# Kernel optimization log

Measured on AMD Instinct MI355X. Metric: run time of the kernel, lower is better.

The kernel has to match this reference:

```python
import jax, jax.numpy as jnp
import numpy as np
import math

B, S, D_MODEL, H, D_K = 8, 1024, 512, 8, 64


def setup_inputs() -> dict:
    key = jax.random.key(0)
    ks = jax.random.split(key, 12)
    s = 1.0 / math.sqrt(D_MODEL)
    inp = {
        "q": jax.random.normal(ks[0], (B, S, D_MODEL), dtype=jnp.float32),
        "k": jax.random.normal(ks[1], (B, S, D_MODEL), dtype=jnp.float32),
        "v": jax.random.normal(ks[2], (B, S, D_MODEL), dtype=jnp.float32),
        "Wq": jax.random.normal(ks[3], (D_MODEL, D_MODEL), dtype=jnp.float32) * s,
        "bq": jnp.zeros((D_MODEL,), dtype=jnp.float32),
        "Wk": jax.random.normal(ks[4], (D_MODEL, D_MODEL), dtype=jnp.float32) * s,
        "bk": jnp.zeros((D_MODEL,), dtype=jnp.float32),
        "Wv": jax.random.normal(ks[5], (D_MODEL, D_MODEL), dtype=jnp.float32) * s,
        "bv": jnp.zeros((D_MODEL,), dtype=jnp.float32),
        "Wo": jax.random.normal(ks[6], (D_MODEL, D_MODEL), dtype=jnp.float32) * s,
        "bo": jnp.zeros((D_MODEL,), dtype=jnp.float32),
        # xavier_uniform on (H,1,1): bound = sqrt(6/(1+1)) ~ 1.732
        "gammas": jax.random.uniform(ks[7], (H, 1, 1), minval=-1.732, maxval=1.732, dtype=jnp.float32),
        "mask": jnp.triu(jnp.ones((S, S), dtype=bool), k=1),  # mask future positions
        "key_padding_mask": jnp.zeros((B, S), dtype=bool),
    }
    return inp


def reference(q, k, v, Wq, bq, Wk, bk, Wv, bv, Wo, bo, gammas, mask, key_padding_mask):
    bs, seqlen = q.shape[0], q.shape[1]
    NEG = -1e32

    def proj(x, W, b):
        # nn.Linear: x @ W.T + b, then split heads -> [b, h, s, d_k]
        return (x @ W.T + b).reshape(bs, seqlen, H, D_K).transpose(0, 2, 1, 3)

    qh, kh, vh = proj(q, Wq, bq), proj(k, Wk, bk), proj(v, Wv, bv)

    scores = jnp.einsum("bhqd,bhkd->bhqk", qh, kh) / math.sqrt(D_K)
    full_mask = mask[None, None, :, :] | key_padding_mask[:, None, None, :]  # [b,1,s,s] bcast over h

    # --- distance-decay branch (torch.no_grad / detach) ---
    scores_ = jax.nn.softmax(jnp.where(full_mask, NEG, scores), axis=-1)
    scores_ = scores_ * (~full_mask).astype(scores.dtype)
    distcum = jnp.cumsum(scores_, axis=-1)  # forward=True
    disttotal = jnp.sum(scores_, axis=-1, keepdims=True)
    idx = jnp.arange(seqlen)
    position_effect = jnp.abs(idx[None, :] - idx[:, None]).astype(scores.dtype)  # |i-j|
    dist_scores = jnp.sqrt(jnp.clip((disttotal - distcum) * position_effect, 0.0))
    dist_scores = jax.lax.stop_gradient(dist_scores)

    gamma = -jax.nn.softplus(gammas)[None]  # [1, h, 1, 1]
    total_effect = jnp.clip(jnp.exp(dist_scores * gamma), 1e-5, 1e5)

    attn = jax.nn.softmax(jnp.where(full_mask, NEG, scores * total_effect), axis=-1)
    out = jnp.einsum("bhqk,bhkd->bhqd", attn, vh)
    concat = out.transpose(0, 2, 1, 3).reshape(bs, seqlen, D_MODEL)
    return concat @ Wo.T + bo
```

## Files before the change

### kernel.cpp

```cpp
#include <hip/hip_runtime.h>
#include <hip/hip_bf16.h>
#include <math.h>

#define NB   8
#define NS   1024
#define NDM  512
#define NH   8
#define NDK  64
#define NM   8192

typedef __attribute__((ext_vector_type(8))) short short8;
typedef __attribute__((ext_vector_type(4))) float f32x4;

__device__ __forceinline__ unsigned short f2b(float f) {
    __hip_bfloat16 h = __float2bfloat16(f);
    unsigned short u;
    __builtin_memcpy(&u, &h, 2);
    return u;
}
__device__ __forceinline__ float b2f(unsigned short u) {
    return __uint_as_float(((unsigned)u) << 16);
}
__device__ __forceinline__ float exp2_raw(float x) { float r; asm("v_exp_f32 %0, %1" : "=v"(r) : "v"(x)); return r; }
__device__ __forceinline__ float sqrt_raw(float x) { float r; asm("v_sqrt_f32 %0, %1" : "=v"(r) : "v"(x)); return r; }
__device__ __forceinline__ float rcp_raw(float x)  { float r; asm("v_rcp_f32 %0, %1" : "=v"(r) : "v"(x)); return r; }

template<int CTRL, int RM>
__device__ __forceinline__ float dpp_mov0(float x) {
    int m = __builtin_amdgcn_update_dpp(0, __float_as_int(x), CTRL, RM, 0xf, true);
    return __int_as_float(m);
}
__device__ __forceinline__ float wave_incl_scan(float x) {
    x += dpp_mov0<0x111, 0xf>(x);
    x += dpp_mov0<0x112, 0xf>(x);
    x += dpp_mov0<0x114, 0xf>(x);
    x += dpp_mov0<0x118, 0xf>(x);
    x += dpp_mov0<0x142, 0xa>(x);
    x += dpp_mov0<0x143, 0xc>(x);
    return x;
}
__device__ __forceinline__ float lane63(float x) {
    return __int_as_float(__builtin_amdgcn_readlane(__float_as_int(x), 63));
}

__device__ __forceinline__ short8 pack8(float4 a, float4 b) {
    short8 r;
    r[0] = (short)f2b(a.x); r[1] = (short)f2b(a.y);
    r[2] = (short)f2b(a.z); r[3] = (short)f2b(a.w);
    r[4] = (short)f2b(b.x); r[5] = (short)f2b(b.y);
    r[6] = (short)f2b(b.z); r[7] = (short)f2b(b.w);
    return r;
}

__device__ __forceinline__ void gload16(const unsigned short* g, unsigned short* l) {
    __builtin_amdgcn_global_load_lds(
        (const __attribute__((address_space(1))) void*)g,
        (__attribute__((address_space(3))) void*)l, 16, 0, 0);
}

template<int OMODE, bool ACVT, bool BCVT>
__device__ __forceinline__ void gemm_body64(unsigned short* As, unsigned short* Bs,
                                            const void* __restrict__ Ap,
                                            const void* __restrict__ Wp,
                                            const float* __restrict__ bias,
                                            void* __restrict__ outp) {
    const int tid = threadIdx.x, lane = tid & 63, wid = tid >> 6;
    const int l15 = lane & 15, lhi = lane >> 4;
    const int m0 = (blockIdx.x >> 2) * 64;
    const int n0 = (blockIdx.x & 3) * 128;
    const int wr = wid >> 1, wc = wid & 1;
    const float* Af = (const float*)Ap;
    const unsigned short* Ab = (const unsigned short*)Ap;
    const float* Wf = (const float*)Wp;
    const unsigned short* Wb = (const unsigned short*)Wp;

    f32x4 acc[2][4];
#pragma unroll
    for (int i = 0; i < 2; ++i)
#pragma unroll
        for (int j = 0; j < 4; ++j) acc[i][j] = (f32x4){0.f, 0.f, 0.f, 0.f};

    for (int kk0 = 0; kk0 < NDM; kk0 += 64) {
#pragma unroll
        for (int c = 0; c < 2; ++c) {
            int ci = tid + 256 * c, row = ci >> 3, ch = ci & 7;
            int sch = ch ^ (row & 7);
            if (ACVT) {
                const float* p = Af + (size_t)(m0 + row) * NDM + kk0 + ch * 8;
                *(short8*)(As + row * 64 + sch * 8) = pack8(*(const float4*)p, *(const float4*)(p + 4));
            } else {
                gload16(Ab + (size_t)(m0 + row) * NDM + kk0 + sch * 8, As + ci * 8);
            }
        }
#pragma unroll
        for (int c = 0; c < 4; ++c) {
            int ci = tid + 256 * c, row = ci >> 3, ch = ci & 7;
            int sch = ch ^ (row & 7);
            if (BCVT) {
                const float* p = Wf + (size_t)(n0 + row) * NDM + kk0 + ch * 8;
                *(short8*)(Bs + row * 64 + sch * 8) = pack8(*(const float4*)p, *(const float4*)(p + 4));
            } else {
                gload16(Wb + (size_t)(n0 + row) * NDM + kk0 + sch * 8, Bs + ci * 8);
            }
        }
        __syncthreads();
        short8 af[2][2], bf[4][2];
#pragma unroll
        for (int mi = 0; mi < 2; ++mi)
#pragma unroll
            for (int kk = 0; kk < 2; ++kk) {
                int row = wr * 32 + mi * 16 + l15;
                af[mi][kk] = *(const short8*)(As + row * 64 + (((kk * 4 + lhi) ^ (l15 & 7)) << 3));
            }
#pragma unroll
        for (int ni = 0; ni < 4; ++ni)
#pragma unroll
            for (int kk = 0; kk < 2; ++kk) {
                int row = wc * 64 + ni * 16 + l15;
                bf[ni][kk] = *(const short8*)(Bs + row * 64 + (((kk * 4 + lhi) ^ (l15 & 7)) << 3));
            }
#pragma unroll
        for (int mi = 0; mi < 2; ++mi)
#pragma unroll
            for (int ni = 0; ni < 4; ++ni) {
                acc[mi][ni] = __builtin_amdgcn_mfma_f32_16x16x32_bf16(af[mi][0], bf[ni][0], acc[mi][ni], 0, 0, 0);
                acc[mi][ni] = __builtin_amdgcn_mfma_f32_16x16x32_bf16(af[mi][1], bf[ni][1], acc[mi][ni], 0, 0, 0);
            }
        __syncthreads();
    }

#pragma unroll
    for (int mi = 0; mi < 2; ++mi) {
#pragma unroll
        for (int ni = 0; ni < 4; ++ni) {
            int row0 = m0 + wr * 32 + mi * 16 + lhi * 4;
            int col  = n0 + wc * 64 + ni * 16 + l15;
            float bv = bias[col];
            if (OMODE == 0) {
                unsigned short* o = (unsigned short*)outp;
                int h = col >> 6, d = col & 63;
#pragma unroll
                for (int r = 0; r < 4; ++r) {
                    int m = row0 + r;
                    int b = m >> 10, s = m & 1023;
                    o[(size_t)(((b * NH + h) * NS) + s) * NDK + d] = f2b(acc[mi][ni][r] + bv);
                }
            } else if (OMODE == 1) {
                unsigned short* o = (unsigned short*)outp;
                int h = col >> 6, d = col & 63;
                int b = row0 >> 10, s0 = row0 & 1023;
                ushort4 u;
                u.x = f2b(acc[mi][ni][0] + bv);
                u.y = f2b(acc[mi][ni][1] + bv);
                u.z = f2b(acc[mi][ni][2] + bv);
                u.w = f2b(acc[mi][ni][3] + bv);
                *(ushort4*)(o + (size_t)((b * NH + h) * NDK + d) * NS + s0) = u;
            } else {
                float* o = (float*)outp;
#pragma unroll
                for (int r = 0; r < 4; ++r)
                    o[(size_t)(row0 + r) * NDM + col] = acc[mi][ni][r] + bv;
            }
        }
    }
}

__global__ __launch_bounds__(256, 4) void qkv_gemm(const float* __restrict__ q,
                                                   const float* __restrict__ k,
                                                   const float* __restrict__ v,
                                                   const float* __restrict__ Wq,
                                                   const float* __restrict__ Wk,
                                                   const float* __restrict__ Wv,
                                                   const float* __restrict__ bq,
                                                   const float* __restrict__ bk,
                                                   const float* __restrict__ bv,
                                                   unsigned short* __restrict__ Qh,
                                                   unsigned short* __restrict__ Kh,
                                                   unsigned short* __restrict__ Vt) {
    __shared__ unsigned short As[64 * 64];
    __shared__ unsigned short Bs[128 * 64];
    const int y = blockIdx.y;
    if (y == 0)      gemm_body64<0, true, true>(As, Bs, q, Wq, bq, Qh);
    else if (y == 1) gemm_body64<0, true, true>(As, Bs, k, Wk, bk, Kh);
    else             gemm_body64<1, true, true>(As, Bs, v, Wv, bv, Vt);
}

__global__ __launch_bounds__(256, 4) void wo_gemm(const unsigned short* __restrict__ A,
                                                  const float* __restrict__ Wo,
                                                  const float* __restrict__ bo,
                                                  float* __restrict__ out) {
    __shared__ unsigned short As[64 * 64];
    __shared__ unsigned short Bs[128 * 64];
    gemm_body64<2, false, true>(As, Bs, A, Wo, bo, out);
}

template<int EW>
__device__ __forceinline__ void phase2_rows(unsigned short* pb, int r0, int wid,
                                            int lane, float g2) {
    const int cb = lane * EW;
#pragma unroll
    for (int t = 0; t < 4; ++t) {
        const int rr = wid + 4 * t;
        const int i  = r0 + rr;
        unsigned short* rowp = pb + rr * 1024;
        float s[EW];
        if (EW == 8) {
            short8 raw = *(const short8*)(rowp + ((lane ^ rr) << 3));
#pragma unroll
            for (int u = 0; u < 8; ++u) s[u] = b2f((unsigned short)raw[u]);
        } else {
            short8 raw0 = *(const short8*)(rowp + (((2 * lane)     ^ rr) << 3));
            short8 raw1 = *(const short8*)(rowp + (((2 * lane + 1) ^ rr) << 3));
#pragma unroll
            for (int u = 0; u < 8; ++u) {
                s[u]     = b2f((unsigned short)raw0[u]);
                s[(EW == 16 ? 8 : 0) + u] = b2f((unsigned short)raw1[u]);
            }
        }
#pragma unroll
        for (int u = 0; u < EW; ++u)
            if (cb + u > i) s[u] = -1e30f;
        float p[EW];
        float run = 0.f;
#pragma unroll
        for (int u = 0; u < EW; ++u) { run += exp2_raw(s[u]); p[u] = run; }
        const float inc      = wave_incl_scan(run);
        const float l1       = lane63(inc);
        const float invl1    = rcp_raw(l1);
        const float taillane = l1 - (inc - run);
        const float di       = (float)(i - cb);
        float l2 = 0.f;
#pragma unroll
        for (int u = 0; u < EW; ++u) {
            float tail = fmaxf(taillane - p[u], 0.f);
            float t2   = (tail * invl1) * (di - (float)u);
            float te   = fmaxf(exp2_raw(g2 * sqrt_raw(t2)), 1e-5f);
            float w    = exp2_raw(s[u] * te);
            s[u] = w;
            l2 += w;
        }
        const float l2t  = lane63(wave_incl_scan(l2));
        const float inv2 = rcp_raw(l2t);
        if (EW == 8) {
            short8 h;
#pragma unroll
            for (int u = 0; u < 8; ++u) h[u] = (short)f2b(s[u] * inv2);
            *(short8*)(rowp + ((lane ^ rr) << 3)) = h;
        } else {
            short8 h0, h1;
#pragma unroll
            for (int u = 0; u < 8; ++u) {
                h0[u] = (short)f2b(s[u] * inv2);
                h1[u] = (short)f2b(s[(EW == 16 ? 8 : 0) + u] * inv2);
            }
            *(short8*)(rowp + (((2 * lane)     ^ rr) << 3)) = h0;
            *(short8*)(rowp + (((2 * lane + 1) ^ rr) << 3)) = h1;
        }
    }
}

__global__ __launch_bounds__(256, 4) void attn_kernel(const unsigned short* __restrict__ Qh,
                                                      const unsigned short* __restrict__ Kh,
                                                      const unsigned short* __restrict__ Vt,
                                                      const float* __restrict__ gammas,
                                                      unsigned short* __restrict__ concat) {
    __shared__ unsigned short pb[16 * 1024];
    const int bh   = blockIdx.x & 63;
    const int pair = blockIdx.x >> 6;
    const int tid = threadIdx.x, lane = tid & 63, wid = tid >> 6;
    const int l15 = lane & 15, lhi = lane >> 4;
    const float SC = 0.125f * 1.44269504f;

    const unsigned short* Kb = Kh + (size_t)bh * NS * NDK;
    const unsigned short* Vb = Vt + (size_t)bh * NDK * NS;
    const float g  = gammas[bh & (NH - 1)];
    const float g2 = -log1pf(__expf(g)) * 1.44269504f;
    const int bq_ = bh >> 3, hq = bh & 7;

    for (int hs = 0; hs < 2; ++hs) {
        const int qt = hs ? (63 - pair) : pair;
        const int r0 = qt * 16;
        const int C  = ((r0 + 16 + 63) >> 6) << 6;

        const unsigned short* Qb = Qh + (size_t)(bh * NS + r0) * NDK;
        short8 qf0 = *(const short8*)(Qb + l15 * NDK + lhi * 8);
        short8 qf1 = *(const short8*)(Qb + l15 * NDK + lhi * 8 + 32);
        for (int j0 = wid * 16; j0 < C; j0 += 64) {
            const unsigned short* kp = Kb + (size_t)(j0 + l15) * NDK + lhi * 8;
            short8 kf0 = *(const short8*)kp;
            short8 kf1 = *(const short8*)(kp + 32);
            f32x4 a = {0.f, 0.f, 0.f, 0.f};
            a = __builtin_amdgcn_mfma_f32_16x16x32_bf16(kf0, qf0, a, 0, 0, 0);
            a = __builtin_amdgcn_mfma_f32_16x16x32_bf16(kf1, qf1, a, 0, 0, 0);
            ushort4 u;
            u.x = f2b(a[0] * SC);
            u.y = f2b(a[1] * SC);
            u.z = f2b(a[2] * SC);
            u.w = f2b(a[3] * SC);
            int ch = ((j0 >> 3) + (lhi >> 1)) ^ l15;
            *(ushort4*)(pb + l15 * 1024 + ch * 8 + (lhi & 1) * 4) = u;
        }
        __syncthreads();

        if (hs == 0) phase2_rows<8>(pb, r0, wid, lane, g2);
        else         phase2_rows<16>(pb, r0, wid, lane, g2);
        __syncthreads();

        const int d0 = wid * 16;
        f32x4 acc = {0.f, 0.f, 0.f, 0.f};
        for (int j0 = 0; j0 < C; j0 += 32) {
            short8 av = *(const short8*)(Vb + (size_t)(d0 + l15) * NS + j0 + lhi * 8);
            short8 pw = *(const short8*)(pb + l15 * 1024 + (((((j0 >> 3) + lhi)) ^ l15) << 3));
            acc = __builtin_amdgcn_mfma_f32_16x16x32_bf16(av, pw, acc, 0, 0, 0);
        }
        {
            int d = d0 + lhi * 4;
            int s = r0 + l15;
            ushort4 u;
            u.x = f2b(acc[0]); u.y = f2b(acc[1]);
            u.z = f2b(acc[2]); u.w = f2b(acc[3]);
            *(ushort4*)(concat + (size_t)(bq_ * NS + s) * NDM + hq * NDK + d) = u;
        }
        __syncthreads();
    }
}

extern "C" void kernel_launch(void* const* d_in, const int* in_sizes, int n_in,
                              void* d_out, int out_size, void* d_ws, size_t ws_size,
                              hipStream_t stream) {
    const float* q  = (const float*)d_in[0];
    const float* k  = (const float*)d_in[1];
    const float* v  = (const float*)d_in[2];
    const float* Wq = (const float*)d_in[3];
    const float* bq = (const float*)d_in[4];
    const float* Wk = (const float*)d_in[5];
    const float* bk = (const float*)d_in[6];
    const float* Wv = (const float*)d_in[7];
    const float* bv = (const float*)d_in[8];
    const float* Wo = (const float*)d_in[9];
    const float* bo = (const float*)d_in[10];
    const float* gm = (const float*)d_in[11];

    char* w = (char*)d_ws;
    unsigned short* Qh     = (unsigned short*)(w);
    unsigned short* Kh     = (unsigned short*)(w + (size_t)8388608);
    unsigned short* Vt     = (unsigned short*)(w + (size_t)16777216);
    unsigned short* concat = (unsigned short*)(w + (size_t)25165824);

    qkv_gemm<<<dim3(512, 3), dim3(256), 0, stream>>>(q, k, v, Wq, Wk, Wv, bq, bk, bv, Qh, Kh, Vt);
    attn_kernel<<<dim3(2048), dim3(256), 0, stream>>>(Qh, Kh, Vt, gm, concat);
    wo_gemm<<<dim3(512), dim3(256), 0, stream>>>(concat, Wo, bo, (float*)d_out);
}
```

Before: 129.8 us.

## Enlarge GEMM tiles to 128x128 and use truncating bf16 conversion

The projection and output GEMMs move from 64x128 to 128x128 block tiles, so each wave computes a 64x64 sub-tile. This halves the grid and raises operand reuse per LDS load, at the cost of more accumulator registers and lower occupancy. All fp32-to-bf16 conversions switch from round-to-nearest to bit truncation with packed 32-bit stores, which cuts conversion ALU work. Truncation adds a small downward bias and extra rounding error in Q/K/V, the probabilities and concat.

```diff
diff --git a/kernel.cpp b/kernel.cpp
--- a/kernel.cpp
+++ b/kernel.cpp
@@ -12,11 +12,11 @@
 typedef __attribute__((ext_vector_type(8))) short short8;
 typedef __attribute__((ext_vector_type(4))) float f32x4;
 
-__device__ __forceinline__ unsigned short f2b(float f) {
-    __hip_bfloat16 h = __float2bfloat16(f);
-    unsigned short u;
-    __builtin_memcpy(&u, &h, 2);
-    return u;
+__device__ __forceinline__ unsigned int pack2t(float lo, float hi) {
+    return (__float_as_uint(hi) & 0xffff0000u) | (__float_as_uint(lo) >> 16);
+}
+__device__ __forceinline__ unsigned short f2bt(float f) {
+    return (unsigned short)(__float_as_uint(f) >> 16);
 }
 __device__ __forceinline__ float b2f(unsigned short u) {
     return __uint_as_float(((unsigned)u) << 16);
@@ -43,12 +43,15 @@
     return __int_as_float(__builtin_amdgcn_readlane(__float_as_int(x), 63));
 }
 
-__device__ __forceinline__ short8 pack8(float4 a, float4 b) {
-    short8 r;
-    r[0] = (short)f2b(a.x); r[1] = (short)f2b(a.y);
-    r[2] = (short)f2b(a.z); r[3] = (short)f2b(a.w);
-    r[4] = (short)f2b(b.x); r[5] = (short)f2b(b.y);
-    r[6] = (short)f2b(b.z); r[7] = (short)f2b(b.w);
+__device__ __forceinline__ uint4 pack8t(const float* p) {
+    const unsigned int* u = (const unsigned int*)p;
+    uint4 a = *(const uint4*)u;
+    uint4 b = *(const uint4*)(u + 4);
+    uint4 r;
+    r.x = (a.y & 0xffff0000u) | (a.x >> 16);
+    r.y = (a.w & 0xffff0000u) | (a.z >> 16);
+    r.z = (b.y & 0xffff0000u) | (b.x >> 16);
+    r.w = (b.w & 0xffff0000u) | (b.z >> 16);
     return r;
 }
 
@@ -59,14 +62,14 @@
 }
 
 template<int OMODE, bool ACVT, bool BCVT>
-__device__ __forceinline__ void gemm_body64(unsigned short* As, unsigned short* Bs,
-                                            const void* __restrict__ Ap,
-                                            const void* __restrict__ Wp,
-                                            const float* __restrict__ bias,
-                                            void* __restrict__ outp) {
+__device__ __forceinline__ void gemm_body128(unsigned short* As, unsigned short* Bs,
+                                             const void* __restrict__ Ap,
+                                             const void* __restrict__ Wp,
+                                             const float* __restrict__ bias,
+                                             void* __restrict__ outp) {
     const int tid = threadIdx.x, lane = tid & 63, wid = tid >> 6;
     const int l15 = lane & 15, lhi = lane >> 4;
-    const int m0 = (blockIdx.x >> 2) * 64;
+    const int m0 = (blockIdx.x >> 2) * 128;
     const int n0 = (blockIdx.x & 3) * 128;
     const int wr = wid >> 1, wc = wid & 1;
     const float* Af = (const float*)Ap;
@@ -74,20 +77,20 @@
     const float* Wf = (const float*)Wp;
     const unsigned short* Wb = (const unsigned short*)Wp;
 
-    f32x4 acc[2][4];
-#pragma unroll
-    for (int i = 0; i < 2; ++i)
+    f32x4 acc[4][4];
+#pragma unroll
+    for (int i = 0; i < 4; ++i)
 #pragma unroll
         for (int j = 0; j < 4; ++j) acc[i][j] = (f32x4){0.f, 0.f, 0.f, 0.f};
 
     for (int kk0 = 0; kk0 < NDM; kk0 += 64) {
 #pragma unroll
-        for (int c = 0; c < 2; ++c) {
+        for (int c = 0; c < 4; ++c) {
             int ci = tid + 256 * c, row = ci >> 3, ch = ci & 7;
             int sch = ch ^ (row & 7);
             if (ACVT) {
                 const float* p = Af + (size_t)(m0 + row) * NDM + kk0 + ch * 8;
-                *(short8*)(As + row * 64 + sch * 8) = pack8(*(const float4*)p, *(const float4*)(p + 4));
+                *(uint4*)(As + row * 64 + sch * 8) = pack8t(p);
             } else {
                 gload16(Ab + (size_t)(m0 + row) * NDM + kk0 + sch * 8, As + ci * 8);
             }
@@ -98,42 +101,39 @@
             int sch = ch ^ (row & 7);
             if (BCVT) {
                 const float* p = Wf + (size_t)(n0 + row) * NDM + kk0 + ch * 8;
-                *(short8*)(Bs + row * 64 + sch * 8) = pack8(*(const float4*)p, *(const float4*)(p + 4));
+                *(uint4*)(Bs + row * 64 + sch * 8) = pack8t(p);
             } else {
                 gload16(Wb + (size_t)(n0 + row) * NDM + kk0 + sch * 8, Bs + ci * 8);
             }
         }
         __syncthreads();
-        short8 af[2][2], bf[4][2];
-#pragma unroll
-        for (int mi = 0; mi < 2; ++mi)
-#pragma unroll
-            for (int kk = 0; kk < 2; ++kk) {
-                int row = wr * 32 + mi * 16 + l15;
-                af[mi][kk] = *(const short8*)(As + row * 64 + (((kk * 4 + lhi) ^ (l15 & 7)) << 3));
-            }
-#pragma unroll
-        for (int ni = 0; ni < 4; ++ni)
-#pragma unroll
-            for (int kk = 0; kk < 2; ++kk) {
+#pragma unroll
+        for (int kk = 0; kk < 2; ++kk) {
+            short8 af[4], bf[4];
+#pragma unroll
+            for (int mi = 0; mi < 4; ++mi) {
+                int row = wr * 64 + mi * 16 + l15;
+                af[mi] = *(const short8*)(As + row * 64 + (((kk * 4 + lhi) ^ (l15 & 7)) << 3));
+            }
+#pragma unroll
+            for (int ni = 0; ni < 4; ++ni) {
                 int row = wc * 64 + ni * 16 + l15;
-                bf[ni][kk] = *(const short8*)(Bs + row * 64 + (((kk * 4 + lhi) ^ (l15 & 7)) << 3));
-            }
-#pragma unroll
-        for (int mi = 0; mi < 2; ++mi)
-#pragma unroll
-            for (int ni = 0; ni < 4; ++ni) {
-                acc[mi][ni] = __builtin_amdgcn_mfma_f32_16x16x32_bf16(af[mi][0], bf[ni][0], acc[mi][ni], 0, 0, 0);
-                acc[mi][ni] = __builtin_amdgcn_mfma_f32_16x16x32_bf16(af[mi][1], bf[ni][1], acc[mi][ni], 0, 0, 0);
-            }
+                bf[ni] = *(const short8*)(Bs + row * 64 + (((kk * 4 + lhi) ^ (l15 & 7)) << 3));
+            }
+#pragma unroll
+            for (int mi = 0; mi < 4; ++mi)
+#pragma unroll
+                for (int ni = 0; ni < 4; ++ni)
+                    acc[mi][ni] = __builtin_amdgcn_mfma_f32_16x16x32_bf16(af[mi], bf[ni], acc[mi][ni], 0, 0, 0);
+        }
         __syncthreads();
     }
 
 #pragma unroll
-    for (int mi = 0; mi < 2; ++mi) {
+    for (int mi = 0; mi < 4; ++mi) {
 #pragma unroll
         for (int ni = 0; ni < 4; ++ni) {
-            int row0 = m0 + wr * 32 + mi * 16 + lhi * 4;
+            int row0 = m0 + wr * 64 + mi * 16 + lhi * 4;
             int col  = n0 + wc * 64 + ni * 16 + l15;
             float bv = bias[col];
             if (OMODE == 0) {
@@ -143,18 +143,16 @@
                 for (int r = 0; r < 4; ++r) {
                     int m = row0 + r;
                     int b = m >> 10, s = m & 1023;
-                    o[(size_t)(((b * NH + h) * NS) + s) * NDK + d] = f2b(acc[mi][ni][r] + bv);
+                    o[(size_t)(((b * NH + h) * NS) + s) * NDK + d] = f2bt(acc[mi][ni][r] + bv);
                 }
             } else if (OMODE == 1) {
                 unsigned short* o = (unsigned short*)outp;
                 int h = col >> 6, d = col & 63;
                 int b = row0 >> 10, s0 = row0 & 1023;
-                ushort4 u;
-                u.x = f2b(acc[mi][ni][0] + bv);
-                u.y = f2b(acc[mi][ni][1] + bv);
-                u.z = f2b(acc[mi][ni][2] + bv);
-                u.w = f2b(acc[mi][ni][3] + bv);
-                *(ushort4*)(o + (size_t)((b * NH + h) * NDK + d) * NS + s0) = u;
+                uint2 pu;
+                pu.x = pack2t(acc[mi][ni][0] + bv, acc[mi][ni][1] + bv);
+                pu.y = pack2t(acc[mi][ni][2] + bv, acc[mi][ni][3] + bv);
+                *(uint2*)(o + (size_t)((b * NH + h) * NDK + d) * NS + s0) = pu;
             } else {
                 float* o = (float*)outp;
 #pragma unroll
@@ -165,33 +163,33 @@
     }
 }
 
-__global__ __launch_bounds__(256, 4) void qkv_gemm(const float* __restrict__ q,
-                                                   const float* __restrict__ k,
-                                                   const float* __restrict__ v,
-                                                   const float* __restrict__ Wq,
-                                                   const float* __restrict__ Wk,
-                                                   const float* __restrict__ Wv,
-                                                   const float* __restrict__ bq,
-                                                   const float* __restrict__ bk,
-                                                   const float* __restrict__ bv,
-                                                   unsigned short* __restrict__ Qh,
-                                                   unsigned short* __restrict__ Kh,
-                                                   unsigned short* __restrict__ Vt) {
-    __shared__ unsigned short As[64 * 64];
+__global__ __launch_bounds__(256) void qkv_gemm(const float* __restrict__ q,
+                                                const float* __restrict__ k,
+                                                const float* __restrict__ v,
+                                                const float* __restrict__ Wq,
+                                                const float* __restrict__ Wk,
+                                                const float* __restrict__ Wv,
+                                                const float* __restrict__ bq,
+                                                const float* __restrict__ bk,
+                                                const float* __restrict__ bv,
+                                                unsigned short* __restrict__ Qh,
+                                                unsigned short* __restrict__ Kh,
+                                                unsigned short* __restrict__ Vt) {
+    __shared__ unsigned short As[128 * 64];
     __shared__ unsigned short Bs[128 * 64];
     const int y = blockIdx.y;
-    if (y == 0)      gemm_body64<0, true, true>(As, Bs, q, Wq, bq, Qh);
-    else if (y == 1) gemm_body64<0, true, true>(As, Bs, k, Wk, bk, Kh);
-    else             gemm_body64<1, true, true>(As, Bs, v, Wv, bv, Vt);
-}
-
-__global__ __launch_bounds__(256, 4) void wo_gemm(const unsigned short* __restrict__ A,
-                                                  const float* __restrict__ Wo,
-                                                  const float* __restrict__ bo,
-                                                  float* __restrict__ out) {
-    __shared__ unsigned short As[64 * 64];
+    if (y == 0)      gemm_body128<0, true, true>(As, Bs, q, Wq, bq, Qh);
+    else if (y == 1) gemm_body128<0, true, true>(As, Bs, k, Wk, bk, Kh);
+    else             gemm_body128<1, true, true>(As, Bs, v, Wv, bv, Vt);
+}
+
+__global__ __launch_bounds__(256) void wo_gemm(const unsigned short* __restrict__ A,
+                                               const float* __restrict__ Wo,
+                                               const float* __restrict__ bo,
+                                               float* __restrict__ out) {
+    __shared__ unsigned short As[128 * 64];
     __shared__ unsigned short Bs[128 * 64];
-    gemm_body64<2, false, true>(As, Bs, A, Wo, bo, out);
+    gemm_body128<2, false, true>(As, Bs, A, Wo, bo, out);
 }
 
 template<int EW>
@@ -242,19 +240,24 @@
         const float l2t  = lane63(wave_incl_scan(l2));
         const float inv2 = rcp_raw(l2t);
         if (EW == 8) {
-            short8 h;
-#pragma unroll
-            for (int u = 0; u < 8; ++u) h[u] = (short)f2b(s[u] * inv2);
-            *(short8*)(rowp + ((lane ^ rr) << 3)) = h;
+            uint4 h;
+            h.x = pack2t(s[0] * inv2, s[1] * inv2);
+            h.y = pack2t(s[2] * inv2, s[3] * inv2);
+            h.z = pack2t(s[4] * inv2, s[5] * inv2);
+            h.w = pack2t(s[6] * inv2, s[7] * inv2);
+            *(uint4*)(rowp + ((lane ^ rr) << 3)) = h;
         } else {
-            short8 h0, h1;
-#pragma unroll
-            for (int u = 0; u < 8; ++u) {
-                h0[u] = (short)f2b(s[u] * inv2);
-                h1[u] = (short)f2b(s[(EW == 16 ? 8 : 0) + u] * inv2);
-            }
-            *(short8*)(rowp + (((2 * lane)     ^ rr) << 3)) = h0;
-            *(short8*)(rowp + (((2 * lane + 1) ^ rr) << 3)) = h1;
+            uint4 h0, h1;
+            h0.x = pack2t(s[0] * inv2, s[1] * inv2);
+            h0.y = pack2t(s[2] * inv2, s[3] * inv2);
+            h0.z = pack2t(s[4] * inv2, s[5] * inv2);
+            h0.w = pack2t(s[6] * inv2, s[7] * inv2);
+            h1.x = pack2t(s[8] * inv2, s[9] * inv2);
+            h1.y = pack2t(s[10] * inv2, s[11] * inv2);
+            h1.z = pack2t(s[12] * inv2, s[13] * inv2);
+            h1.w = pack2t(s[14] * inv2, s[15] * inv2);
+            *(uint4*)(rowp + (((2 * lane)     ^ rr) << 3)) = h0;
+            *(uint4*)(rowp + (((2 * lane + 1) ^ rr) << 3)) = h1;
         }
     }
 }
@@ -292,13 +295,11 @@
             f32x4 a = {0.f, 0.f, 0.f, 0.f};
             a = __builtin_amdgcn_mfma_f32_16x16x32_bf16(kf0, qf0, a, 0, 0, 0);
             a = __builtin_amdgcn_mfma_f32_16x16x32_bf16(kf1, qf1, a, 0, 0, 0);
-            ushort4 u;
-            u.x = f2b(a[0] * SC);
-            u.y = f2b(a[1] * SC);
-            u.z = f2b(a[2] * SC);
-            u.w = f2b(a[3] * SC);
+            uint2 pu;
+            pu.x = pack2t(a[0] * SC, a[1] * SC);
+            pu.y = pack2t(a[2] * SC, a[3] * SC);
             int ch = ((j0 >> 3) + (lhi >> 1)) ^ l15;
-            *(ushort4*)(pb + l15 * 1024 + ch * 8 + (lhi & 1) * 4) = u;
+            *(uint2*)(pb + l15 * 1024 + ch * 8 + (lhi & 1) * 4) = pu;
         }
         __syncthreads();
 
@@ -316,10 +317,10 @@
         {
             int d = d0 + lhi * 4;
             int s = r0 + l15;
-            ushort4 u;
-            u.x = f2b(acc[0]); u.y = f2b(acc[1]);
-            u.z = f2b(acc[2]); u.w = f2b(acc[3]);
-            *(ushort4*)(concat + (size_t)(bq_ * NS + s) * NDM + hq * NDK + d) = u;
+            uint2 pu;
+            pu.x = pack2t(acc[0], acc[1]);
+            pu.y = pack2t(acc[2], acc[3]);
+            *(uint2*)(concat + (size_t)(bq_ * NS + s) * NDM + hq * NDK + d) = pu;
         }
         __syncthreads();
     }
@@ -347,7 +348,7 @@
     unsigned short* Vt     = (unsigned short*)(w + (size_t)16777216);
     unsigned short* concat = (unsigned short*)(w + (size_t)25165824);
 
-    qkv_gemm<<<dim3(512, 3), dim3(256), 0, stream>>>(q, k, v, Wq, Wk, Wv, bq, bk, bv, Qh, Kh, Vt);
+    qkv_gemm<<<dim3(256, 3), dim3(256), 0, stream>>>(q, k, v, Wq, Wk, Wv, bq, bk, bv, Qh, Kh, Vt);
     attn_kernel<<<dim3(2048), dim3(256), 0, stream>>>(Qh, Kh, Vt, gm, concat);
-    wo_gemm<<<dim3(512), dim3(256), 0, stream>>>(concat, Wo, bo, (float*)d_out);
-}
+    wo_gemm<<<dim3(256), dim3(256), 0, stream>>>(concat, Wo, bo, (float*)d_out);
+}
```

Result: slower. 133.8 us (+3.1%).
